# Performance work log

Hardware: AMD Instinct MI355X
Metric: run time of the kernel (lower is better)

Reference implementation:

```python
import jax, jax.numpy as jnp
import numpy as np
from jax import lax

B, Hm, Wm = 8, 128, 128          # batch, mesh height, mesh width
DIM, HEADS, DH, G, K = 128, 8, 64, 64, 3
INNER = HEADS * DH
N = Hm * Wm


def setup_inputs() -> dict:
    key = jax.random.key(0)
    ks = jax.random.split(key, 12)
    s = 0.02
    x = jax.random.normal(ks[0], (B, N, DIM), dtype=jnp.float32)
    conv_fx_w = jax.random.normal(ks[1], (K, K, DIM, INNER), dtype=jnp.float32) * s
    conv_fx_b = jnp.zeros((INNER,), dtype=jnp.float32)
    conv_x_w = jax.random.normal(ks[2], (K, K, DIM, INNER), dtype=jnp.float32) * s
    conv_x_b = jnp.zeros((INNER,), dtype=jnp.float32)
    # nn.Linear(dim_head, slice_num): weight (G, DH), orthogonal-init approximated by scaled normal
    slice_w = jax.random.normal(ks[3], (G, DH), dtype=jnp.float32) * (1.0 / np.sqrt(DH))
    slice_b = jnp.zeros((G,), dtype=jnp.float32)
    temperature = jnp.ones((1, HEADS, 1, 1), dtype=jnp.float32) * 0.5
    wq = jax.random.normal(ks[4], (DH, DH), dtype=jnp.float32) * s
    wk = jax.random.normal(ks[5], (DH, DH), dtype=jnp.float32) * s
    wv = jax.random.normal(ks[6], (DH, DH), dtype=jnp.float32) * s
    out_w = jax.random.normal(ks[7], (DIM, INNER), dtype=jnp.float32) * s
    out_b = jnp.zeros((DIM,), dtype=jnp.float32)
    return {
        "x": x,
        "conv_fx_w": conv_fx_w, "conv_fx_b": conv_fx_b,
        "conv_x_w": conv_x_w, "conv_x_b": conv_x_b,
        "slice_w": slice_w, "slice_b": slice_b,
        "temperature": temperature,
        "wq": wq, "wk": wk, "wv": wv,
        "out_w": out_w, "out_b": out_b,
    }


def _conv(z, w, b):
    # z: (B, H, W, Cin); w: (K, K, Cin, Cout); SAME padding, stride 1
    return lax.conv_general_dilated(
        z, w, window_strides=(1, 1), padding="SAME",
        dimension_numbers=("NHWC", "HWIO", "NHWC")) + b


def reference(x, conv_fx_w, conv_fx_b, conv_x_w, conv_x_b,
              slice_w, slice_b, temperature, wq, wk, wv, out_w, out_b):
    b, n, c = x.shape
    xi = x.reshape(b, Hm, Wm, c)
    # (B,H,W,INNER) -> (B,N,heads,dh) -> (B,heads,N,dh)
    fx_mid = _conv(xi, conv_fx_w, conv_fx_b).reshape(b, n, HEADS, DH).transpose(0, 2, 1, 3)
    x_mid = _conv(xi, conv_x_w, conv_x_b).reshape(b, n, HEADS, DH).transpose(0, 2, 1, 3)

    temp = jnp.clip(temperature, 0.1, 5.0)  # (1,heads,1,1)
    logits = (jnp.einsum("bhnc,gc->bhng", x_mid, slice_w) + slice_b) / temp
    slice_weights = jax.nn.softmax(logits, axis=-1)         # (B,heads,N,G)

    slice_norm = slice_weights.sum(axis=2)                   # (B,heads,G)
    slice_token = jnp.einsum("bhnc,bhng->bhgc", fx_mid, slice_weights)
    slice_token = slice_token / (slice_norm + 1e-5)[..., None]

    q = jnp.einsum("bhgc,dc->bhgd", slice_token, wq)
    k = jnp.einsum("bhgc,dc->bhgd", slice_token, wk)
    v = jnp.einsum("bhgc,dc->bhgd", slice_token, wv)

    scale = DH ** (-0.5)
    attn = jax.nn.softmax(jnp.einsum("bhgd,bhkd->bhgk", q, k) * scale, axis=-1)
    out_slice = jnp.einsum("bhgk,bhkd->bhgd", attn, v)       # (B,heads,G,dh)

    out_x = jnp.einsum("bhgc,bhng->bhnc", out_slice, slice_weights)
    out_x = out_x.transpose(0, 2, 1, 3).reshape(b, n, INNER)
    return jnp.einsum("bnc,dc->bnd", out_x, out_w) + out_b
```

## Files before the change

### kernel.cpp

```cpp
#include <hip/hip_runtime.h>
#include <stdint.h>

#define BATCH 8
#define HEADS 8
#define HM 128
#define WM 128
#define NPIX (HM*WM)
#define DIMC 128
#define DH 64
#define GS 64
#define INNER 512
#define KTOT 1152
#define XT_LD 128

typedef unsigned short u16;
typedef short v8s __attribute__((ext_vector_type(8)));
typedef float v4f __attribute__((ext_vector_type(4)));

__device__ __forceinline__ u16 f2bf(float f) {
    unsigned x = __float_as_uint(f);
    return (u16)((x + 0x7fffu + ((x >> 16) & 1u)) >> 16);
}
__device__ __forceinline__ float bf2f(u16 u) { return __uint_as_float(((unsigned)u) << 16); }
__device__ __forceinline__ unsigned cvtpk(float lo, float hi) {
    unsigned r;
    asm("v_cvt_pk_bf16_f32 %0, %1, %2" : "=v"(r) : "v"(lo), "v"(hi));
    return r;
}

union BF8 { uint4 v; u16 s[8]; };

__global__ __launch_bounds__(256) void k_build_w(
    const float* __restrict__ wx, const float* __restrict__ wfx,
    const float* __restrict__ slw, const float* __restrict__ temp,
    u16* __restrict__ wcatT, u16* __restrict__ wfxT)
{
    __shared__ float sw_l[GS][DH + 1];
    __shared__ float wx_l[INNER];
    int row = blockIdx.x;
    int t = threadIdx.x;
    for (int i = t; i < GS * DH; i += 256) sw_l[i >> 6][i & 63] = slw[i];
    for (int i = t; i < INNER; i += 256) wx_l[i] = wx[(size_t)row * INNER + i];
    __syncthreads();
#pragma unroll
    for (int j = 0; j < 2; j++) {
        int co = j * 256 + t;
        int h = co >> 6, g = co & 63;
        float s = 0.f;
        for (int c = 0; c < DH; c++) s = fmaf(wx_l[h * 64 + c], sw_l[g][c], s);
        float tv = fminf(fmaxf(temp[h], 0.1f), 5.0f);
        wcatT[(size_t)co * KTOT + row] = f2bf(s / tv);
        wfxT[(size_t)co * KTOT + row] = f2bf(wfx[(size_t)row * INNER + co]);
    }
}

__global__ __launch_bounds__(512) void k_build_b(
    const float* __restrict__ bx, const float* __restrict__ slw,
    const float* __restrict__ slb, const float* __restrict__ temp,
    float* __restrict__ bcatL)
{
    int co = threadIdx.x;
    int h = co >> 6, g = co & 63;
    float s = slb[g];
    for (int c = 0; c < DH; c++) s = fmaf(bx[h * 64 + c], slw[g * 64 + c], s);
    float tv = fminf(fmaxf(temp[h], 0.1f), 5.0f);
    bcatL[co] = s / tv;
}

union SmemC {
    u16 X[66 * XT_LD];
    struct { u16 SwT[64][64]; u16 FxT[64][64]; } e;
};

__global__ __launch_bounds__(256, 4) void k_conv2(
    const float* __restrict__ xin, const u16* __restrict__ wcatT,
    const u16* __restrict__ wfxT, const float* __restrict__ bcatL,
    const float* __restrict__ bfx, u16* __restrict__ swbT,
    float* __restrict__ straw, float* __restrict__ norm)
{
    __shared__ SmemC sm;
    int bid = blockIdx.x;
    int swz = (bid & 7) * 1024 + (bid >> 3);
    int b = swz >> 10;
    int r = swz & 1023;
    int y = r >> 3, half = (r >> 2) & 1, ct = r & 3;
    int cob = ct << 7;
    int t = threadIdx.x;
    int lane = t & 63, wave = t >> 6;
    int w_conv = wave >> 1, w_co = wave & 1;
    int l16 = lane & 15, lk = lane >> 4;

    v4f acc[4][4];
#pragma unroll
    for (int i = 0; i < 4; i++)
#pragma unroll
        for (int j = 0; j < 4; j++) acc[i][j] = v4f{0.f, 0.f, 0.f, 0.f};

    const u16* wT = w_conv ? wfxT : wcatT;
    const u16* wrb[4];
#pragma unroll
    for (int nj = 0; nj < 4; nj++)
        wrb[nj] = wT + (size_t)(cob + w_co * 64 + nj * 16 + l16) * KTOT + lk * 8;

#pragma unroll
    for (int ky = 0; ky < 3; ky++) {
        int yy = y + ky - 1;
        bool yok = (unsigned)yy < (unsigned)HM;
        const float* xrow = xin + ((size_t)b * NPIX + (size_t)yy * WM) * DIMC;
        if (ky) __syncthreads();
#pragma unroll
        for (int it = 0; it < 5; it++) {
            int i = t + it * 256;
            if (i < 1056) {
                int row = i >> 4, k8 = i & 15;
                int px = half * 64 + row - 1;
                uint4 o;
                if (yok && (unsigned)px < (unsigned)WM) {
                    const float4* p = (const float4*)(xrow + (size_t)px * DIMC + k8 * 8);
                    float4 fa = p[0], fb = p[1];
                    o = make_uint4(cvtpk(fa.x, fa.y), cvtpk(fa.z, fa.w),
                                   cvtpk(fb.x, fb.y), cvtpk(fb.z, fb.w));
                } else {
                    o = make_uint4(0u, 0u, 0u, 0u);
                }
                *(uint4*)(sm.X + row * XT_LD + ((k8 ^ (row & 7)) * 8)) = o;
            }
        }
        __syncthreads();
#pragma unroll
        for (int cc = 0; cc < 12; cc++) {
            int kx = cc >> 2, c4 = cc & 3;
            int wo = (ky * 3 + kx) * 128 + c4 * 32;
            v8s bB[4];
#pragma unroll
            for (int nj = 0; nj < 4; nj++)
                bB[nj] = *(const v8s*)(wrb[nj] + wo);
            int xr7 = (l16 + kx) & 7;
            const u16* xb = sm.X + (l16 + kx) * XT_LD;
            int xo = (((c4 * 4 + lk) ^ xr7) * 8);
            v8s av[4];
#pragma unroll
            for (int mi = 0; mi < 4; mi++)
                av[mi] = *(const v8s*)(xb + mi * 16 * XT_LD + xo);
#pragma unroll
            for (int mi = 0; mi < 4; mi++)
#pragma unroll
                for (int nj = 0; nj < 4; nj++)
                    acc[mi][nj] = __builtin_amdgcn_mfma_f32_16x16x32_bf16(
                        av[mi], bB[nj], acc[mi][nj], 0, 0, 0);
        }
    }
    __syncthreads();

    float bb[4];
#pragma unroll
    for (int nj = 0; nj < 4; nj++)
        bb[nj] = (w_conv ? bfx : bcatL)[cob + w_co * 64 + nj * 16 + l16];

    if (w_conv == 0) {
#pragma unroll
        for (int mi = 0; mi < 4; mi++) {
#pragma unroll
            for (int q = 0; q < 4; q++) {
                float m = acc[mi][0][q] + bb[0];
#pragma unroll
                for (int nj = 1; nj < 4; nj++) m = fmaxf(m, acc[mi][nj][q] + bb[nj]);
                m = fmaxf(m, __shfl_xor(m, 1));
                m = fmaxf(m, __shfl_xor(m, 2));
                m = fmaxf(m, __shfl_xor(m, 4));
                m = fmaxf(m, __shfl_xor(m, 8));
                float ssum = 0.f;
#pragma unroll
                for (int nj = 0; nj < 4; nj++) {
                    float e = __expf(acc[mi][nj][q] + bb[nj] - m);
                    acc[mi][nj][q] = e; ssum += e;
                }
                ssum += __shfl_xor(ssum, 1);
                ssum += __shfl_xor(ssum, 2);
                ssum += __shfl_xor(ssum, 4);
                ssum += __shfl_xor(ssum, 8);
                float inv = 1.f / ssum;
#pragma unroll
                for (int nj = 0; nj < 4; nj++) acc[mi][nj][q] *= inv;
            }
        }
#pragma unroll
        for (int nj = 0; nj < 4; nj++) {
            float pn = 0.f;
#pragma unroll
            for (int mi = 0; mi < 4; mi++)
#pragma unroll
                for (int q = 0; q < 4; q++) pn += acc[mi][nj][q];
            pn += __shfl_xor(pn, 16);
            pn += __shfl_xor(pn, 32);
            if (lk == 0)
                atomicAdd(&norm[(size_t)(b * HEADS + 2 * ct + w_co) * GS + nj * 16 + l16], pn);
        }
    }

#pragma unroll
    for (int hp = 0; hp < 2; hp++) {
        bool mine = (w_co == hp);
        if (mine) {
#pragma unroll
            for (int nj = 0; nj < 4; nj++) {
                int grow = nj * 16 + l16;
                int r7 = l16 & 7;
#pragma unroll
                for (int mi = 0; mi < 4; mi++) {
                    int off = (((mi * 2 + (lk >> 1)) ^ r7) * 8) + (lk & 1) * 4;
                    uint2 wv;
                    if (w_conv == 0) {
                        wv.x = cvtpk(acc[mi][nj][0], acc[mi][nj][1]);
                        wv.y = cvtpk(acc[mi][nj][2], acc[mi][nj][3]);
                        *(uint2*)&sm.e.SwT[grow][off] = wv;
                    } else {
                        wv.x = cvtpk(acc[mi][nj][0] + bb[nj], acc[mi][nj][1] + bb[nj]);
                        wv.y = cvtpk(acc[mi][nj][2] + bb[nj], acc[mi][nj][3] + bb[nj]);
                        *(uint2*)&sm.e.FxT[grow][off] = wv;
                    }
                }
            }
        }
        __syncthreads();
        if (mine) {
            v4f pacc[2][4];
#pragma unroll
            for (int i = 0; i < 2; i++)
#pragma unroll
                for (int j = 0; j < 4; j++) pacc[i][j] = v4f{0.f, 0.f, 0.f, 0.f};
            int r7 = l16 & 7;
#pragma unroll
            for (int c = 0; c < 2; c++) {
                int ko = (((c * 4 + lk) ^ r7) * 8);
                v8s aw[2], bw[4];
#pragma unroll
                for (int mi = 0; mi < 2; mi++)
                    aw[mi] = *(const v8s*)(&sm.e.SwT[w_conv * 32 + mi * 16 + l16][0] + ko);
#pragma unroll
                for (int nj = 0; nj < 4; nj++)
                    bw[nj] = *(const v8s*)(&sm.e.FxT[nj * 16 + l16][0] + ko);
#pragma unroll
                for (int mi = 0; mi < 2; mi++)
#pragma unroll
                    for (int nj = 0; nj < 4; nj++)
                        pacc[mi][nj] = __builtin_amdgcn_mfma_f32_16x16x32_bf16(
                            aw[mi], bw[nj], pacc[mi][nj], 0, 0, 0);
            }
            int bh2 = b * HEADS + 2 * ct + hp;
#pragma unroll
            for (int mi = 0; mi < 2; mi++)
#pragma unroll
                for (int nj = 0; nj < 4; nj++)
#pragma unroll
                    for (int q = 0; q < 4; q++) {
                        int g = w_conv * 32 + mi * 16 + lk * 4 + q;
                        int dh = nj * 16 + l16;
                        atomicAdd(&straw[((size_t)bh2 * GS + g) * DH + dh], pacc[mi][nj][q]);
                    }
        }
#pragma unroll
        for (int it = 0; it < 2; it++) {
            int chunk = it * 256 + t;
            int gi = chunk >> 3;
            int p8 = chunk & 7;
            uint4 v = *(const uint4*)(&sm.e.SwT[gi][0] + ((p8 ^ (gi & 7)) * 8));
            size_t di = (((size_t)(b * HEADS + 2 * ct + hp) * GS + gi) * NPIX)
                        + (size_t)y * WM + half * 64 + p8 * 8;
            *(uint4*)&swbT[di] = v;
        }
        __syncthreads();
    }
}

__global__ __launch_bounds__(256) void k_attn(
    const float* __restrict__ straw, const float* __restrict__ norm,
    const float* __restrict__ wq, const float* __restrict__ wk, const float* __restrict__ wv,
    const float* __restrict__ outw, float* __restrict__ m1)
{
    __shared__ float lds[4][64][64];
    int bh = blockIdx.x, h = bh & 7;
    int t = threadIdx.x;
    for (int i = t; i < 4096; i += 256) {
        int g = i >> 6;
        lds[0][g][i & 63] = straw[(size_t)bh * 4096 + i] / (norm[bh * 64 + g] + 1e-5f);
    }
    __syncthreads();
    int g = t >> 2, d0 = (t & 3) << 4;
    for (int d = d0; d < d0 + 16; d++) {
        float sq = 0.f, sk = 0.f, sv = 0.f;
        for (int c = 0; c < 64; c++) {
            float sc = lds[0][g][c];
            sq = fmaf(sc, wq[d * 64 + c], sq);
            sk = fmaf(sc, wk[d * 64 + c], sk);
            sv = fmaf(sc, wv[d * 64 + c], sv);
        }
        lds[1][g][d] = sq; lds[2][g][d] = sk; lds[3][g][d] = sv;
    }
    __syncthreads();
    float attnrow[16];
    for (int k2 = d0, i = 0; k2 < d0 + 16; k2++, i++) {
        float s = 0.f;
        for (int d = 0; d < 64; d++) s = fmaf(lds[1][g][d], lds[2][k2][d], s);
        attnrow[i] = s * 0.125f;
    }
    __syncthreads();
    for (int i = 0; i < 16; i++) lds[0][g][d0 + i] = attnrow[i];
    __syncthreads();
    if (t < 64) {
        float mx = -1e30f;
        for (int j = 0; j < 64; j++) mx = fmaxf(mx, lds[0][t][j]);
        float s = 0.f;
        for (int j = 0; j < 64; j++) { float e = __expf(lds[0][t][j] - mx); lds[0][t][j] = e; s += e; }
        float inv = 1.f / s;
        for (int j = 0; j < 64; j++) lds[0][t][j] *= inv;
    }
    __syncthreads();
    float osrow[16];
    for (int d = d0, i = 0; d < d0 + 16; d++, i++) {
        float s = 0.f;
        for (int kx = 0; kx < 64; kx++) s = fmaf(lds[0][g][kx], lds[3][kx][d], s);
        osrow[i] = s;
    }
    __syncthreads();
    for (int i = 0; i < 16; i++) lds[2][g][d0 + i] = osrow[i];
    __syncthreads();
    int dimb = (t & 3) << 5;
    for (int dim = dimb; dim < dimb + 32; dim++) {
        float s = 0.f;
        for (int c = 0; c < 64; c++)
            s = fmaf(lds[2][g][c], outw[(size_t)dim * INNER + h * 64 + c], s);
        m1[((size_t)bh * 64 + g) * DIMC + dim] = s;
    }
}

__global__ __launch_bounds__(256) void k_final(
    const u16* __restrict__ swbT, const float* __restrict__ m1,
    const float* __restrict__ outb, float* __restrict__ out)
{
    __shared__ float As[32][68];
    __shared__ float Bs[32][128];
    int b = blockIdx.x, nt = blockIdx.y;
    int t = threadIdx.x;
    int tn = t & 15, tm = t >> 4;
    float acc[4][8];
#pragma unroll
    for (int i = 0; i < 4; i++)
#pragma unroll
        for (int j = 0; j < 8; j++) acc[i][j] = 0.f;
    int n0 = nt * 64;
    int gg = t >> 3, nq = (t & 7) * 8;
    int g2 = t >> 3, dd = (t & 7) * 16;
    for (int h = 0; h < HEADS; h++) {
        const u16* swp = swbT + (size_t)(b * HEADS + h) * GS * NPIX;
        const float* m1p = m1 + (size_t)(b * HEADS + h) * GS * DIMC;
        for (int g0 = 0; g0 < 64; g0 += 32) {
            __syncthreads();
            BF8 av8; av8.v = *(const uint4*)&swp[(size_t)(g0 + gg) * NPIX + n0 + nq];
#pragma unroll
            for (int i = 0; i < 8; i++) As[gg][nq + i] = bf2f(av8.s[i]);
            const float* bp = m1p + (size_t)(g0 + g2) * DIMC + dd;
            *(float4*)&Bs[g2][dd + 0]  = *(const float4*)(bp + 0);
            *(float4*)&Bs[g2][dd + 4]  = *(const float4*)(bp + 4);
            *(float4*)&Bs[g2][dd + 8]  = *(const float4*)(bp + 8);
            *(float4*)&Bs[g2][dd + 12] = *(const float4*)(bp + 12);
            __syncthreads();
#pragma unroll
            for (int kk = 0; kk < 32; kk++) {
                float4 a = *(const float4*)&As[kk][tm * 4];
                float4 b0 = *(const float4*)&Bs[kk][tn * 4];
                float4 b1 = *(const float4*)&Bs[kk][tn * 4 + 64];
                float av[4] = {a.x, a.y, a.z, a.w};
                float bv[8] = {b0.x, b0.y, b0.z, b0.w, b1.x, b1.y, b1.z, b1.w};
#pragma unroll
                for (int i = 0; i < 4; i++)
#pragma unroll
                    for (int j = 0; j < 8; j++)
                        acc[i][j] = fmaf(av[i], bv[j], acc[i][j]);
            }
        }
    }
    float4 bias0 = *(const float4*)&outb[tn * 4];
    float4 bias1 = *(const float4*)&outb[64 + tn * 4];
#pragma unroll
    for (int i = 0; i < 4; i++) {
        size_t n = (size_t)n0 + tm * 4 + i;
        size_t rb = ((size_t)b * NPIX + n) * DIMC;
        float4 r0, r1;
        r0.x = acc[i][0] + bias0.x; r0.y = acc[i][1] + bias0.y;
        r0.z = acc[i][2] + bias0.z; r0.w = acc[i][3] + bias0.w;
        r1.x = acc[i][4] + bias1.x; r1.y = acc[i][5] + bias1.y;
        r1.z = acc[i][6] + bias1.z; r1.w = acc[i][7] + bias1.w;
        *(float4*)&out[rb + tn * 4] = r0;
        *(float4*)&out[rb + 64 + tn * 4] = r1;
    }
}

extern "C" void kernel_launch(void* const* d_in, const int* in_sizes, int n_in,
                              void* d_out, int out_size, void* d_ws, size_t ws_size,
                              hipStream_t stream)
{
    (void)in_sizes; (void)n_in; (void)out_size;
    const float* x    = (const float*)d_in[0];
    const float* wfx  = (const float*)d_in[1];
    const float* bfx  = (const float*)d_in[2];
    const float* wx   = (const float*)d_in[3];
    const float* bx   = (const float*)d_in[4];
    const float* slw  = (const float*)d_in[5];
    const float* slb  = (const float*)d_in[6];
    const float* temp = (const float*)d_in[7];
    const float* wq   = (const float*)d_in[8];
    const float* wk   = (const float*)d_in[9];
    const float* wv   = (const float*)d_in[10];
    const float* outw = (const float*)d_in[11];
    const float* outb = (const float*)d_in[12];
    float* out = (float*)d_out;
    float* W = (float*)d_ws;

    u16*   wcatT = (u16*)W;
    u16*   wfxT  = (u16*)(W + 294912);
    float* bcatL = W + 589824;
    float* norm  = W + 590336;
    float* straw = W + 594432;
    float* m1    = W + 856576;
    u16*   swbT  = (u16*)(W + 1380864);
    const size_t need = 1380864ull * 4 + 67108864ull * 2;
    if (ws_size < need) return;

    hipMemsetAsync(norm, 0, (4096 + 262144) * sizeof(float), stream);

    k_build_w<<<dim3(1152), 256, 0, stream>>>(wx, wfx, slw, temp, wcatT, wfxT);
    k_build_b<<<dim3(1), 512, 0, stream>>>(bx, slw, slb, temp, bcatL);
    k_conv2<<<dim3(8192), 256, 0, stream>>>(x, wcatT, wfxT, bcatL, bfx, swbT, straw, norm);
    k_attn<<<dim3(64), 256, 0, stream>>>(straw, norm, wq, wk, wv, outw, m1);
    k_final<<<dim3(8, 256), 256, 0, stream>>>(swbT, m1, outb, out);
}
```

Baseline: 1.228 ms.

## Retile conv kernel to full-row per head with double-buffered weight loads

Each conv block now covers a full 128-pixel row for one head instead of half a row for two heads. Waves split by pixel half and conv type rather than by output-channel half. This halves the atomicAdd traffic on straw/norm per pixel, removes the two-pass head loop and its extra barriers, and double-buffers the weight fragment loads from global memory a step ahead. In exchange LDS use doubles (a 130-row input tile) and launch bounds drop to 3 blocks per CU, which lowers occupancy.

```diff
diff --git a/kernel.cpp b/kernel.cpp
--- a/kernel.cpp
+++ b/kernel.cpp
@@ -68,11 +68,11 @@
 }
 
 union SmemC {
-    u16 X[66 * XT_LD];
-    struct { u16 SwT[64][64]; u16 FxT[64][64]; } e;
+    u16 X[130 * XT_LD];
+    struct { u16 SwT[64][128]; u16 FxT[64][128]; } e;
 };
 
-__global__ __launch_bounds__(256, 4) void k_conv2(
+__global__ __launch_bounds__(256, 3) void k_conv2(
     const float* __restrict__ xin, const u16* __restrict__ wcatT,
     const u16* __restrict__ wfxT, const float* __restrict__ bcatL,
     const float* __restrict__ bfx, u16* __restrict__ swbT,
@@ -83,12 +83,13 @@
     int swz = (bid & 7) * 1024 + (bid >> 3);
     int b = swz >> 10;
     int r = swz & 1023;
-    int y = r >> 3, half = (r >> 2) & 1, ct = r & 3;
-    int cob = ct << 7;
+    int y = r >> 3, h = r & 7;
+    int cob = h << 6;
     int t = threadIdx.x;
     int lane = t & 63, wave = t >> 6;
-    int w_conv = wave >> 1, w_co = wave & 1;
+    int half = wave >> 1, w_conv = wave & 1;
     int l16 = lane & 15, lk = lane >> 4;
+    int bh = b * HEADS + h;
 
     v4f acc[4][4];
 #pragma unroll
@@ -100,7 +101,11 @@
     const u16* wrb[4];
 #pragma unroll
     for (int nj = 0; nj < 4; nj++)
-        wrb[nj] = wT + (size_t)(cob + w_co * 64 + nj * 16 + l16) * KTOT + lk * 8;
+        wrb[nj] = wT + (size_t)(cob + nj * 16 + l16) * KTOT + lk * 8;
+
+    v8s bB[2][4];
+#pragma unroll
+    for (int nj = 0; nj < 4; nj++) bB[0][nj] = *(const v8s*)(wrb[nj]);
 
 #pragma unroll
     for (int ky = 0; ky < 3; ky++) {
@@ -109,11 +114,11 @@
         const float* xrow = xin + ((size_t)b * NPIX + (size_t)yy * WM) * DIMC;
         if (ky) __syncthreads();
 #pragma unroll
-        for (int it = 0; it < 5; it++) {
+        for (int it = 0; it < 9; it++) {
             int i = t + it * 256;
-            if (i < 1056) {
+            if (i < 2080) {
                 int row = i >> 4, k8 = i & 15;
-                int px = half * 64 + row - 1;
+                int px = row - 1;
                 uint4 o;
                 if (yok && (unsigned)px < (unsigned)WM) {
                     const float4* p = (const float4*)(xrow + (size_t)px * DIMC + k8 * 8);
@@ -129,14 +134,15 @@
         __syncthreads();
 #pragma unroll
         for (int cc = 0; cc < 12; cc++) {
+            int gidx = ky * 12 + cc;
+            if (gidx < 35) {
+#pragma unroll
+                for (int nj = 0; nj < 4; nj++)
+                    bB[(gidx + 1) & 1][nj] = *(const v8s*)(wrb[nj] + (gidx + 1) * 32);
+            }
             int kx = cc >> 2, c4 = cc & 3;
-            int wo = (ky * 3 + kx) * 128 + c4 * 32;
-            v8s bB[4];
-#pragma unroll
-            for (int nj = 0; nj < 4; nj++)
-                bB[nj] = *(const v8s*)(wrb[nj] + wo);
             int xr7 = (l16 + kx) & 7;
-            const u16* xb = sm.X + (l16 + kx) * XT_LD;
+            const u16* xb = sm.X + (half * 64 + l16 + kx) * XT_LD;
             int xo = (((c4 * 4 + lk) ^ xr7) * 8);
             v8s av[4];
 #pragma unroll
@@ -147,7 +153,7 @@
 #pragma unroll
                 for (int nj = 0; nj < 4; nj++)
                     acc[mi][nj] = __builtin_amdgcn_mfma_f32_16x16x32_bf16(
-                        av[mi], bB[nj], acc[mi][nj], 0, 0, 0);
+                        av[mi], bB[gidx & 1][nj], acc[mi][nj], 0, 0, 0);
         }
     }
     __syncthreads();
@@ -155,7 +161,7 @@
     float bb[4];
 #pragma unroll
     for (int nj = 0; nj < 4; nj++)
-        bb[nj] = (w_conv ? bfx : bcatL)[cob + w_co * 64 + nj * 16 + l16];
+        bb[nj] = (w_conv ? bfx : bcatL)[cob + nj * 16 + l16];
 
     if (w_conv == 0) {
 #pragma unroll
@@ -194,82 +200,70 @@
             pn += __shfl_xor(pn, 16);
             pn += __shfl_xor(pn, 32);
             if (lk == 0)
-                atomicAdd(&norm[(size_t)(b * HEADS + 2 * ct + w_co) * GS + nj * 16 + l16], pn);
-        }
-    }
-
-#pragma unroll
-    for (int hp = 0; hp < 2; hp++) {
-        bool mine = (w_co == hp);
-        if (mine) {
+                atomicAdd(&norm[(size_t)bh * GS + nj * 16 + l16], pn);
+        }
+    }
+
+#pragma unroll
+    for (int nj = 0; nj < 4; nj++) {
+        int grow = nj * 16 + l16;
+        int r7 = l16 & 7;
+#pragma unroll
+        for (int mi = 0; mi < 4; mi++) {
+            int p8 = half * 8 + mi * 2 + (lk >> 1);
+            int off = ((p8 ^ r7) * 8) + (lk & 1) * 4;
+            uint2 wv;
+            if (w_conv == 0) {
+                wv.x = cvtpk(acc[mi][nj][0], acc[mi][nj][1]);
+                wv.y = cvtpk(acc[mi][nj][2], acc[mi][nj][3]);
+                *(uint2*)&sm.e.SwT[grow][off] = wv;
+            } else {
+                wv.x = cvtpk(acc[mi][nj][0] + bb[nj], acc[mi][nj][1] + bb[nj]);
+                wv.y = cvtpk(acc[mi][nj][2] + bb[nj], acc[mi][nj][3] + bb[nj]);
+                *(uint2*)&sm.e.FxT[grow][off] = wv;
+            }
+        }
+    }
+    __syncthreads();
+
+    {
+        v4f pacc[4];
+#pragma unroll
+        for (int j = 0; j < 4; j++) pacc[j] = v4f{0.f, 0.f, 0.f, 0.f};
+        int ga = wave * 16 + l16;
+        int ra = ga & 7;
+#pragma unroll
+        for (int c = 0; c < 4; c++) {
+            v8s aw = *(const v8s*)(&sm.e.SwT[ga][0] + (((c * 4 + lk) ^ ra) * 8));
+            v8s bw[4];
 #pragma unroll
             for (int nj = 0; nj < 4; nj++) {
-                int grow = nj * 16 + l16;
-                int r7 = l16 & 7;
-#pragma unroll
-                for (int mi = 0; mi < 4; mi++) {
-                    int off = (((mi * 2 + (lk >> 1)) ^ r7) * 8) + (lk & 1) * 4;
-                    uint2 wv;
-                    if (w_conv == 0) {
-                        wv.x = cvtpk(acc[mi][nj][0], acc[mi][nj][1]);
-                        wv.y = cvtpk(acc[mi][nj][2], acc[mi][nj][3]);
-                        *(uint2*)&sm.e.SwT[grow][off] = wv;
-                    } else {
-                        wv.x = cvtpk(acc[mi][nj][0] + bb[nj], acc[mi][nj][1] + bb[nj]);
-                        wv.y = cvtpk(acc[mi][nj][2] + bb[nj], acc[mi][nj][3] + bb[nj]);
-                        *(uint2*)&sm.e.FxT[grow][off] = wv;
-                    }
-                }
-            }
-        }
-        __syncthreads();
-        if (mine) {
-            v4f pacc[2][4];
-#pragma unroll
-            for (int i = 0; i < 2; i++)
-#pragma unroll
-                for (int j = 0; j < 4; j++) pacc[i][j] = v4f{0.f, 0.f, 0.f, 0.f};
-            int r7 = l16 & 7;
-#pragma unroll
-            for (int c = 0; c < 2; c++) {
-                int ko = (((c * 4 + lk) ^ r7) * 8);
-                v8s aw[2], bw[4];
-#pragma unroll
-                for (int mi = 0; mi < 2; mi++)
-                    aw[mi] = *(const v8s*)(&sm.e.SwT[w_conv * 32 + mi * 16 + l16][0] + ko);
-#pragma unroll
-                for (int nj = 0; nj < 4; nj++)
-                    bw[nj] = *(const v8s*)(&sm.e.FxT[nj * 16 + l16][0] + ko);
-#pragma unroll
-                for (int mi = 0; mi < 2; mi++)
-#pragma unroll
-                    for (int nj = 0; nj < 4; nj++)
-                        pacc[mi][nj] = __builtin_amdgcn_mfma_f32_16x16x32_bf16(
-                            aw[mi], bw[nj], pacc[mi][nj], 0, 0, 0);
-            }
-            int bh2 = b * HEADS + 2 * ct + hp;
-#pragma unroll
-            for (int mi = 0; mi < 2; mi++)
-#pragma unroll
-                for (int nj = 0; nj < 4; nj++)
-#pragma unroll
-                    for (int q = 0; q < 4; q++) {
-                        int g = w_conv * 32 + mi * 16 + lk * 4 + q;
-                        int dh = nj * 16 + l16;
-                        atomicAdd(&straw[((size_t)bh2 * GS + g) * DH + dh], pacc[mi][nj][q]);
-                    }
-        }
-#pragma unroll
-        for (int it = 0; it < 2; it++) {
-            int chunk = it * 256 + t;
-            int gi = chunk >> 3;
-            int p8 = chunk & 7;
-            uint4 v = *(const uint4*)(&sm.e.SwT[gi][0] + ((p8 ^ (gi & 7)) * 8));
-            size_t di = (((size_t)(b * HEADS + 2 * ct + hp) * GS + gi) * NPIX)
-                        + (size_t)y * WM + half * 64 + p8 * 8;
-            *(uint4*)&swbT[di] = v;
-        }
-        __syncthreads();
+                int dr = nj * 16 + l16;
+                bw[nj] = *(const v8s*)(&sm.e.FxT[dr][0] + (((c * 4 + lk) ^ (dr & 7)) * 8));
+            }
+#pragma unroll
+            for (int nj = 0; nj < 4; nj++)
+                pacc[nj] = __builtin_amdgcn_mfma_f32_16x16x32_bf16(
+                    aw, bw[nj], pacc[nj], 0, 0, 0);
+        }
+#pragma unroll
+        for (int nj = 0; nj < 4; nj++)
+#pragma unroll
+            for (int q = 0; q < 4; q++) {
+                int g = wave * 16 + lk * 4 + q;
+                int dh = nj * 16 + l16;
+                atomicAdd(&straw[((size_t)bh * GS + g) * DH + dh], pacc[nj][q]);
+            }
+    }
+
+#pragma unroll
+    for (int it = 0; it < 4; it++) {
+        int chunk = it * 256 + t;
+        int gi = chunk >> 4;
+        int p8 = chunk & 15;
+        uint4 v = *(const uint4*)(&sm.e.SwT[gi][0] + ((p8 ^ (gi & 7)) * 8));
+        size_t di = (((size_t)bh * GS + gi) * NPIX) + (size_t)y * WM + p8 * 8;
+        *(uint4*)&swbT[di] = v;
     }
 }
 
```

Result: faster. 1.162 ms (-5.4%).
